# Kernel tuning notes

Hardware: AMD Instinct MI355X
Metric: run time of the kernel (lower is better)

Reference implementation:

```python
import jax, jax.numpy as jnp
import numpy as np

GELU = lambda x: jax.nn.gelu(x, approximate=False)  # torch nn.GELU default (erf)
BN_EPS = 1e-5

def _conv(x, w, pad):
    return jax.lax.conv_general_dilated(x, w, (1, 1), pad,
                                        dimension_numbers=('NCHW', 'OIHW', 'NCHW'))

def setup_inputs() -> dict:
    B, D, L = 4096, 768, 3
    IC, R = D // 2, 16  # FDA intermediate channels, reduction ratio
    ks = iter(jax.random.split(jax.random.key(0), 64))
    def nrm(shape, s=0.02):
        return jax.random.normal(next(ks), shape, jnp.float32) * s
    z = lambda *s: jnp.zeros(s, jnp.float32)
    o = lambda *s: jnp.ones(s, jnp.float32)
    inp = {
        'text_feature': jax.random.normal(next(ks), (B, D), jnp.float32),
        'image_feature': jax.random.normal(next(ks), (B, D), jnp.float32),
        'tl_w': nrm((D, D)), 'tl_b': z(D),
        'il_w': nrm((D, D)), 'il_b': z(D),
        'sda_wq': nrm((512, D)), 'sda_bq': z(512),
        'sda_wk': nrm((512, D)), 'sda_bk': z(512),
        'sda_wv': nrm((512, D)), 'sda_bv': z(512),
        'sda_wo': nrm((D, 512)), 'sda_bo': z(D),
        'fda_w1': nrm((IC, D, 3, 3)), 'fda_b1': z(IC),
        'fda_bn1_g': o(IC), 'fda_bn1_b': z(IC),
        'fda_ca_w1': nrm((IC // R, IC, 1, 1)), 'fda_ca_w2': nrm((IC, IC // R, 1, 1)),
        'fda_sa_w': nrm((1, IC, 7, 7)), 'fda_sa_b': z(1),
        'fda_dec_w': nrm((1, IC, 1, 1)), 'fda_dec_b': z(1),
        'fda_sigma': jnp.full((1, IC, 1, 1), 1e-5, jnp.float32),
        'fda_wf': nrm((D, IC, 1, 1)), 'fda_bf': z(D),
        'fda_bn2_g': o(D), 'fda_bn2_b': z(D),
        'dmi_wq': nrm((D, D)), 'dmi_bq': z(D),
        'dmi_wk': nrm((D, D)), 'dmi_bk': z(D),
        'dmi_wv': nrm((D, D)), 'dmi_bv': z(D),
        'tg_w1': nrm((D, D)), 'tg_b1': z(D),
        'tg_w2': nrm((D, D)), 'tg_b2': z(D),
        'ig_w1': nrm((D, D)), 'ig_b1': z(D),
        'ig_w2': nrm((D, D)), 'ig_b2': z(D),
        'text_scale': o(1, D), 'image_scale': o(1, D),
        'cls_w': nrm((L, D)), 'cls_b': z(L),
    }
    return inp

def reference(text_feature, image_feature, tl_w, tl_b, il_w, il_b,
              sda_wq, sda_bq, sda_wk, sda_bk, sda_wv, sda_bv, sda_wo, sda_bo,
              fda_w1, fda_b1, fda_bn1_g, fda_bn1_b, fda_ca_w1, fda_ca_w2,
              fda_sa_w, fda_sa_b, fda_dec_w, fda_dec_b, fda_sigma,
              fda_wf, fda_bf, fda_bn2_g, fda_bn2_b,
              dmi_wq, dmi_bq, dmi_wk, dmi_bk, dmi_wv, dmi_bv,
              tg_w1, tg_b1, tg_w2, tg_b2, ig_w1, ig_b1, ig_w2, ig_b2,
              text_scale, image_scale, cls_w, cls_b):
    B, D = text_feature.shape
    H, DK = 8, 64
    # text/image projections (+GELU; dropout is identity at inference)
    t = GELU(text_feature @ tl_w.T + tl_b)
    im = GELU(image_feature @ il_w.T + il_b)
    # SDA multi-head self-attention on text, seq len 1
    q = (t @ sda_wq.T + sda_bq).reshape(B, 1, H, DK).transpose(0, 2, 1, 3)  # [B,H,1,DK]
    k = (t @ sda_wk.T + sda_bk).reshape(B, 1, H, DK).transpose(0, 2, 1, 3)
    v = (t @ sda_wv.T + sda_bv).reshape(B, 1, H, DK).transpose(0, 2, 1, 3)
    att = jax.nn.softmax(jnp.einsum('bhqd,bhkd->bhqk', q, k) / jnp.sqrt(jnp.float32(DK)), -1)
    t = jnp.einsum('bhqk,bhkd->bhqd', att, v).transpose(0, 2, 1, 3).reshape(B, H * DK) @ sda_wo.T + sda_bo
    # FDA on image feature viewed as [B,C,1,1]
    bnscale = 1.0 / jnp.sqrt(1.0 + BN_EPS)  # BN eval mode, running_mean=0, running_var=1
    x = im[:, :, None, None]
    x = _conv(x, fda_w1, ((1, 1), (1, 1))) + fda_b1[None, :, None, None]
    x = GELU(x * bnscale * fda_bn1_g[None, :, None, None] + fda_bn1_b[None, :, None, None])
    ca = jnp.mean(x, axis=(2, 3), keepdims=True)  # AdaptiveAvgPool2d(1)
    ca = GELU(_conv(ca, fda_ca_w1, ((0, 0), (0, 0))))
    ca = jax.nn.sigmoid(_conv(ca, fda_ca_w2, ((0, 0), (0, 0))))
    x = x * ca
    sa = jax.nn.sigmoid(_conv(x, fda_sa_w, ((3, 3), (3, 3))) + fda_sa_b[None, :, None, None])
    x = x * sa
    xg = GELU(_conv(x, fda_dec_w, ((0, 0), (0, 0))) + fda_dec_b[None, :, None, None])  # [B,1,1,1]
    x = x + fda_sigma * (x - xg)  # feat_decompose residual with learned sigma
    x = _conv(x, fda_wf, ((0, 0), (0, 0))) + fda_bf[None, :, None, None]
    x = GELU(x * bnscale * fda_bn2_g[None, :, None, None] + fda_bn2_b[None, :, None, None])
    im = x[:, :, 0, 0]

    def dmi(q_in, kv_in, gw1, gb1, gw2, gb2, scale):
        qp = q_in @ dmi_wq.T + dmi_bq
        kp = kv_in @ dmi_wk.T + dmi_bk
        vp = kv_in @ dmi_wv.T + dmi_bv
        # cross-batch attention: scores are [B,B]
        a = jax.nn.softmax(qp @ kp.T / jnp.sqrt(jnp.float32(D)), -1) @ vp
        # gate Sequential ends in Sigmoid, then forward applies sigmoid AGAIN (faithful)
        gate = jax.nn.sigmoid(jax.nn.relu(a @ gw1.T + gb1) @ gw2.T + gb2)
        return jax.nn.sigmoid(gate) * a * scale

    ct = dmi(t, im, tg_w1, tg_b1, tg_w2, tg_b2, text_scale)
    ci = dmi(im, t, ig_w1, ig_b1, ig_w2, ig_b2, image_scale)
    logits = (ct + ci) @ cls_w.T + cls_b
    return jax.nn.softmax(logits, -1)
```

## Files before the change

### kernel.cpp

```cpp
#include <hip/hip_runtime.h>
#include <hip/hip_bf16.h>
#include <math.h>

typedef __hip_bfloat16 bf16;
typedef __bf16 bf16x8 __attribute__((ext_vector_type(8)));
typedef float f32x4 __attribute__((ext_vector_type(4)));
typedef unsigned short u16;
typedef u16 u16x8 __attribute__((ext_vector_type(8)));

#define NB 4096
#define DM 768

__device__ __forceinline__ float cvt(float x){ return x; }
__device__ __forceinline__ float cvt(bf16 x){ return __bfloat162float(x); }
__device__ __forceinline__ void stv(float* p, float v){ *p = v; }
__device__ __forceinline__ void stv(bf16* p, float v){ *p = __float2bfloat16(v); }

__device__ __forceinline__ float gelu_f(float x){
    return 0.5f * x * (1.0f + erff(x * 0.70710678118654752440f));
}
__device__ __forceinline__ float sigmoid_f(float x){
    return 1.0f / (1.0f + __expf(-x));
}

__device__ __forceinline__ void async_copy16(const void* g, void* l){
    __builtin_amdgcn_global_load_lds((const __attribute__((address_space(1))) void*)g,
                                     (__attribute__((address_space(3))) void*)l, 16, 0, 0);
}

#define MAXJ 8
struct Job {
    const bf16* A; const bf16* B; bf16* C;
    const float* b0; const float* gv; const float* b1;
    float* rs;
    const bf16* aux; const float* sv;
    int M, N, K, ldA, ldB, act, trans, blk0, nx, nb;
    float alpha;
};
struct Jobs { Job j[MAXJ]; int nj; };

__global__ __launch_bounds__(256) void mgemm_k(Jobs jb)
{
    int z = 0;
    #pragma unroll
    for (int i = 1; i < MAXJ; ++i)
        if (i < jb.nj && (int)blockIdx.x >= jb.j[i].blk0) z = i;
    const Job& J = jb.j[z];
    const bf16* __restrict__ A  = J.A;
    const bf16* __restrict__ Bm = J.B;
    bf16* __restrict__ C        = J.C;
    const int bx0 = (int)blockIdx.x - J.blk0;
    int bx = bx0;
    if (J.nx <= 16 && (J.nb & 7) == 0){ const int cpx = J.nb >> 3; bx = (bx0 & 7) * cpx + (bx0 >> 3); }
    const int gx = bx % J.nx;
    const int gy = bx / J.nx;
    const int M = J.M, N = J.N, K = J.K, ldA = J.ldA, ldB = J.ldB;

    __shared__ __align__(16) bf16 smem[17408];
    const int tid  = threadIdx.x;
    const int wave = tid >> 6;
    const int lane = tid & 63;
    const int row0 = gy * 128;
    const int col0 = gx * 128;
    const int wrow = (wave & 1) * 64;
    const int wcol = (wave >> 1) * 64;
    const int fl   = lane & 15;
    const int q    = lane >> 4;

    const int sr8 = lane >> 3;
    const int sc8 = (((lane & 7) ^ sr8)) * 8;
    const bf16* pA = A  + (size_t)(row0 + wave * 32 + sr8) * ldA + sc8;
    const bf16* pB = Bm + (size_t)(col0 + wave * 32 + sr8) * ldB + sc8;
    bf16* ldsA = &smem[(wave * 32) * 64];
    bf16* ldsB = &smem[8192 + (wave * 32) * 64];

    f32x4 acc[4][4] = {};
    for (int k0 = 0; k0 < K; k0 += 64){
        #pragma unroll
        for (int i = 0; i < 4; ++i){
            async_copy16(pA + (size_t)(i * 8) * ldA, ldsA + i * 512);
            async_copy16(pB + (size_t)(i * 8) * ldB, ldsB + i * 512);
        }
        pA += 64; pB += 64;
        __syncthreads();
        #pragma unroll
        for (int ks = 0; ks < 2; ++ks){
            bf16x8 af[4], bfv[4];
            #pragma unroll
            for (int i = 0; i < 4; ++i){
                const int ra = wrow + i * 16 + fl;
                const int rb = wcol + i * 16 + fl;
                const int ca = ((ks * 4 + q) ^ (ra & 7)) * 8;
                const int cb = ((ks * 4 + q) ^ (rb & 7)) * 8;
                af[i]  = *(const bf16x8*)&smem[ra * 64 + ca];
                bfv[i] = *(const bf16x8*)&smem[8192 + rb * 64 + cb];
            }
            #pragma unroll
            for (int mi = 0; mi < 4; ++mi)
                #pragma unroll
                for (int ni = 0; ni < 4; ++ni)
                    acc[mi][ni] = __builtin_amdgcn_mfma_f32_16x16x32_bf16(af[mi], bfv[ni], acc[mi][ni], 0, 0, 0);
        }
        __syncthreads();
    }

    constexpr int ELD = 136;
    #pragma unroll
    for (int ni = 0; ni < 4; ++ni){
        const int col = col0 + wcol + ni * 16 + fl;
        const float b0 = J.b0 ? J.b0[col] : 0.f;
        const float gm = (J.gv ? J.gv[col] : 1.f) * J.alpha;
        const float b1 = J.b1 ? J.b1[col] : 0.f;
        const int lcol = wcol + ni * 16 + fl;
        #pragma unroll
        for (int mi = 0; mi < 4; ++mi){
            const int lrow = wrow + mi * 16 + q * 4;
            #pragma unroll
            for (int r = 0; r < 4; ++r){
                float v = (acc[mi][ni][r] + b0) * gm + b1;
                if      (J.act == 1) v = gelu_f(v);
                else if (J.act == 2) v = sigmoid_f(v);
                else if (J.act == 3) v = fmaxf(v, 0.f);
                else if (J.act == 4) v = __expf(v);
                if (J.trans) smem[(size_t)lcol * ELD + lrow + r] = __float2bfloat16(v);
                else         smem[(size_t)(lrow + r) * ELD + lcol] = __float2bfloat16(v);
            }
        }
    }
    __syncthreads();
    const int erow = tid >> 4;
    const int ecol = (tid & 15) * 8;
    #pragma unroll
    for (int p = 0; p < 8; ++p){
        const int row = p * 16 + erow;
        u16x8 uv = *(const u16x8*)&smem[row * ELD + ecol];
        if (J.act == 5){
            const u16x8 av = *(const u16x8*)((const u16*)J.aux + (size_t)(row0 + row) * N + col0 + ecol);
            #pragma unroll
            for (int j = 0; j < 8; ++j){
                const float g = __uint_as_float((unsigned)uv[j] << 16);
                const float a = __uint_as_float((unsigned)av[j] << 16);
                const float v = sigmoid_f(g) * a * J.sv[col0 + ecol + j];
                uv[j] = __bfloat16_as_ushort(__float2bfloat16(v));
            }
        }
        if (J.trans) *(u16x8*)&C[(size_t)(col0 + row) * M + row0 + ecol] = uv;
        else         *(u16x8*)&C[(size_t)(row0 + row) * N + col0 + ecol] = uv;
        if (J.rs){
            float s = 0.f;
            #pragma unroll
            for (int j = 0; j < 8; ++j) s += __uint_as_float((unsigned)uv[j] << 16);
            s += __shfl_down(s, 8, 16);
            s += __shfl_down(s, 4, 16);
            s += __shfl_down(s, 2, 16);
            s += __shfl_down(s, 1, 16);
            if ((tid & 15) == 0) J.rs[(size_t)gx * M + row0 + row] = s;
        }
    }
}

__global__ __launch_bounds__(256) void denom_k(const float* __restrict__ part, float* __restrict__ l)
{
    const int t = blockIdx.x * 256 + threadIdx.x;
    if (t >= 2 * NB) return;
    const int dir = t >> 12, row = t & (NB - 1);
    const float* p = part + (size_t)dir * 32 * NB + row;
    float s = 0.f;
    #pragma unroll
    for (int c = 0; c < 32; ++c) s += p[(size_t)c * NB];
    l[t] = s;
}

#define NCVT 14
struct CvtDesc { const float* s[NCVT]; bf16* d[NCVT]; int n[NCVT]; };
__global__ __launch_bounds__(256) void cvt_k(CvtDesc cd,
    const float* __restrict__ w1, const float* __restrict__ saw,
    bf16* __restrict__ w1c, float* __restrict__ sac,
    const float* __restrict__ bq, const float* __restrict__ bk,
    float* __restrict__ qkb)
{
    const int e = blockIdx.y;
    if (e == NCVT){
        const int idx = blockIdx.x * 256 + threadIdx.x;
        if (idx < 384 * 768){
            const int oc = idx / 768, ic = idx % 768;
            w1c[idx] = __float2bfloat16(w1[(size_t)oc * 6912 + (size_t)ic * 9 + 4]);
        }
        if (idx < 384) sac[idx] = saw[(size_t)idx * 49 + 24];
        if (idx < 768)                   qkb[idx] = bq[idx];
        else if (idx < 1536)             qkb[idx] = bk[idx - 768];
        return;
    }
    const int base = (blockIdx.x * 256 + threadIdx.x) * 4;
    if (base >= cd.n[e]) return;
    const float4 v = *(const float4*)(cd.s[e] + base);
    union { bf16 h[4]; unsigned long long u; } o;
    o.h[0] = __float2bfloat16(v.x);
    o.h[1] = __float2bfloat16(v.y);
    o.h[2] = __float2bfloat16(v.z);
    o.h[3] = __float2bfloat16(v.w);
    *(unsigned long long*)(cd.d[e] + base) = o.u;
}

__global__ __launch_bounds__(128) void fda_fused_k(
    bf16* __restrict__ x, const float* __restrict__ wc1, const float* __restrict__ wc2,
    const float* __restrict__ sac, const float* __restrict__ sab,
    const float* __restrict__ decw, const float* __restrict__ decb,
    const float* __restrict__ sigma)
{
    __shared__ float xs[384];
    __shared__ float ca1s[24];
    __shared__ float red[128];
    const int b = blockIdx.x;
    const int tid = threadIdx.x;
    bf16* xr = x + (size_t)b * 384;
    #pragma unroll
    for (int i = 0; i < 3; ++i) xs[tid + i * 128] = cvt(xr[tid + i * 128]);
    __syncthreads();
    if (tid < 96){
        const int o = tid >> 2, sub = tid & 3;
        const float* w = wc1 + (size_t)o * 384 + sub * 96;
        float p = 0.f;
        #pragma unroll 8
        for (int k = 0; k < 96; ++k) p = fmaf(xs[sub * 96 + k], w[k], p);
        p += __shfl_down(p, 1, 64);
        p += __shfl_down(p, 2, 64);
        if (sub == 0) ca1s[o] = gelu_f(p);
    }
    __syncthreads();
    float x2[3];
    float p = 0.f;
    #pragma unroll
    for (int i = 0; i < 3; ++i){
        const int c = tid + i * 128;
        float s = 0.f;
        const float* w = wc2 + (size_t)c * 24;
        #pragma unroll
        for (int k = 0; k < 24; ++k) s = fmaf(ca1s[k], w[k], s);
        const float v = xs[c] * sigmoid_f(s);
        x2[i] = v;
        p += v * sac[c];
    }
    red[tid] = p; __syncthreads();
    for (int s = 64; s > 0; s >>= 1){ if (tid < s) red[tid] += red[tid + s]; __syncthreads(); }
    const float sa = sigmoid_f(red[0] + sab[0]);
    __syncthreads();
    float qq = 0.f;
    #pragma unroll
    for (int i = 0; i < 3; ++i){
        const int c = tid + i * 128;
        x2[i] *= sa;
        qq += x2[i] * decw[c];
    }
    red[tid] = qq; __syncthreads();
    for (int s = 64; s > 0; s >>= 1){ if (tid < s) red[tid] += red[tid + s]; __syncthreads(); }
    const float xg = gelu_f(red[0] + decb[0]);
    #pragma unroll
    for (int i = 0; i < 3; ++i){
        const int c = tid + i * 128;
        const float sg = sigma[c];
        stv(&xr[c], x2[i] + sg * (x2[i] - xg));
    }
}

__global__ __launch_bounds__(256) void reduce2_k(
    const bf16* __restrict__ a, const bf16* __restrict__ b, bf16* __restrict__ o1,
    const float* __restrict__ l1,
    const bf16* __restrict__ c, const bf16* __restrict__ d, bf16* __restrict__ o2,
    const float* __restrict__ l2)
{
    const size_t i = ((size_t)blockIdx.x * 256 + threadIdx.x) * 8;
    if (i >= (size_t)NB * DM) return;
    const int row = (int)(i / DM);
    const float inv1 = 1.0f / l1[row];
    const float inv2 = 1.0f / l2[row];
    u16x8 ua = *(const u16x8*)((const u16*)a + i);
    u16x8 ub = *(const u16x8*)((const u16*)b + i);
    u16x8 uc = *(const u16x8*)((const u16*)c + i);
    u16x8 ud = *(const u16x8*)((const u16*)d + i);
    u16x8 r1, r2;
    #pragma unroll
    for (int j = 0; j < 8; ++j){
        const float s1 = (__uint_as_float((unsigned)ua[j] << 16) + __uint_as_float((unsigned)ub[j] << 16)) * inv1;
        const float s2 = (__uint_as_float((unsigned)uc[j] << 16) + __uint_as_float((unsigned)ud[j] << 16)) * inv2;
        r1[j] = __bfloat16_as_ushort(__float2bfloat16(s1));
        r2[j] = __bfloat16_as_ushort(__float2bfloat16(s2));
    }
    *(u16x8*)((u16*)o1 + i) = r1;
    *(u16x8*)((u16*)o2 + i) = r2;
}

__global__ __launch_bounds__(256) void combine_cls_k(
    const bf16* __restrict__ v1, const bf16* __restrict__ v2,
    const float* __restrict__ w, const float* __restrict__ bias, float* __restrict__ out)
{
    __shared__ float r0[256], r1[256], r2[256];
    const int b = blockIdx.x;
    const int tid = threadIdx.x;
    const size_t off = (size_t)b * DM;
    float p0 = 0.f, p1 = 0.f, p2 = 0.f;
    #pragma unroll
    for (int i = 0; i < 3; ++i){
        const int c = tid + i * 256;
        const float v = cvt(v1[off + c]) + cvt(v2[off + c]);
        p0 = fmaf(v, w[c],         p0);
        p1 = fmaf(v, w[DM + c],    p1);
        p2 = fmaf(v, w[2*DM + c],  p2);
    }
    r0[tid] = p0; r1[tid] = p1; r2[tid] = p2; __syncthreads();
    for (int s = 128; s > 0; s >>= 1){
        if (tid < s){ r0[tid] += r0[tid + s]; r1[tid] += r1[tid + s]; r2[tid] += r2[tid + s]; }
        __syncthreads();
    }
    if (tid == 0){
        const float l0 = r0[0] + bias[0];
        const float l1 = r1[0] + bias[1];
        const float l2 = r2[0] + bias[2];
        const float mx = fmaxf(l0, fmaxf(l1, l2));
        const float e0 = __expf(l0 - mx), e1 = __expf(l1 - mx), e2 = __expf(l2 - mx);
        const float inv = 1.f / (e0 + e1 + e2);
        out[(size_t)b * 3 + 0] = e0 * inv;
        out[(size_t)b * 3 + 1] = e1 * inv;
        out[(size_t)b * 3 + 2] = e2 * inv;
    }
}

extern "C" void kernel_launch(void* const* d_in, const int* in_sizes, int n_in,
                              void* d_out, int out_size, void* d_ws, size_t ws_size,
                              hipStream_t stream)
{
    const float* text   = (const float*)d_in[0];
    const float* image  = (const float*)d_in[1];
    const float* tl_w   = (const float*)d_in[2];
    const float* tl_b   = (const float*)d_in[3];
    const float* il_w   = (const float*)d_in[4];
    const float* il_b   = (const float*)d_in[5];
    const float* sda_wv = (const float*)d_in[10];
    const float* sda_bv = (const float*)d_in[11];
    const float* sda_wo = (const float*)d_in[12];
    const float* sda_bo = (const float*)d_in[13];
    const float* fda_w1 = (const float*)d_in[14];
    const float* fda_b1 = (const float*)d_in[15];
    const float* bn1_g  = (const float*)d_in[16];
    const float* bn1_b  = (const float*)d_in[17];
    const float* ca_w1  = (const float*)d_in[18];
    const float* ca_w2  = (const float*)d_in[19];
    const float* sa_w   = (const float*)d_in[20];
    const float* sa_b   = (const float*)d_in[21];
    const float* dec_w  = (const float*)d_in[22];
    const float* dec_b  = (const float*)d_in[23];
    const float* sigma  = (const float*)d_in[24];
    const float* fda_wf = (const float*)d_in[25];
    const float* fda_bf = (const float*)d_in[26];
    const float* bn2_g  = (const float*)d_in[27];
    const float* bn2_b  = (const float*)d_in[28];
    const float* dmi_wq = (const float*)d_in[29];
    const float* dmi_bq = (const float*)d_in[30];
    const float* dmi_wk = (const float*)d_in[31];
    const float* dmi_bk = (const float*)d_in[32];
    const float* dmi_wv = (const float*)d_in[33];
    const float* dmi_bv = (const float*)d_in[34];
    const float* tg_w1  = (const float*)d_in[35];
    const float* tg_b1  = (const float*)d_in[36];
    const float* tg_w2  = (const float*)d_in[37];
    const float* tg_b2  = (const float*)d_in[38];
    const float* ig_w1  = (const float*)d_in[39];
    const float* ig_b1  = (const float*)d_in[40];
    const float* ig_w2  = (const float*)d_in[41];
    const float* ig_b2  = (const float*)d_in[42];
    const float* t_scale= (const float*)d_in[43];
    const float* i_scale= (const float*)d_in[44];
    const float* cls_w  = (const float*)d_in[45];
    const float* cls_b  = (const float*)d_in[46];
    float* out = (float*)d_out;

    char* base = (char*)d_ws;
    auto alloc = [&](size_t bytes){ void* p = (void*)base; base += (bytes + 255) & ~(size_t)255; return p; };
    const size_t SLOT = (size_t)NB * DM;
    const size_t W768 = (size_t)768 * 768;
    bf16* tl_wb   = (bf16*)alloc(W768 * 2);
    bf16* il_wb   = (bf16*)alloc(W768 * 2);
    bf16* sda_wvb = (bf16*)alloc((size_t)512 * 768 * 2);
    bf16* sda_wob = (bf16*)alloc((size_t)768 * 512 * 2);
    bf16* fda_wfb = (bf16*)alloc((size_t)768 * 384 * 2);
    bf16* dmi_wqb = (bf16*)alloc(W768 * 2);
    bf16* dmi_wkb = (bf16*)alloc(W768 * 2);
    bf16* dmi_wvb = (bf16*)alloc(W768 * 2);
    bf16* tg_w1b  = (bf16*)alloc(W768 * 2);
    bf16* tg_w2b  = (bf16*)alloc(W768 * 2);
    bf16* ig_w1b  = (bf16*)alloc(W768 * 2);
    bf16* ig_w2b  = (bf16*)alloc(W768 * 2);
    bf16* w1c     = (bf16*)alloc((size_t)384 * 768 * 2);
    float* sac    = (float*)alloc(1536 * 4);
    float* qkb    = (float*)alloc(1536 * 4);
    float* lbuf   = (float*)alloc(2 * NB * 4);
    float* part   = (float*)alloc((size_t)2 * 32 * NB * 4);
    bf16* SL[8];
    for (int i = 0; i < 8; ++i) SL[i] = (bf16*)alloc(SLOT * 2);
    bf16* SC1 = (bf16*)alloc((size_t)NB * NB * 2);
    bf16* SC2 = (bf16*)alloc((size_t)NB * NB * 2);

    const float bnscale = 1.0f / sqrtf(1.0f + 1e-5f);
    const float iscale  = 1.0f / sqrtf(768.0f);
    const dim3 blk(256);

    struct JB {
        Jobs jb; int blocks;
        void add(const bf16* A, const bf16* B, bf16* C, int M, int N, int K, int ldA, int ldB,
                 const float* b0, float al, const float* gv, const float* b1, int act, int trans,
                 float* rs = nullptr, const bf16* aux = nullptr, const float* sv = nullptr){
            Job& j = jb.j[jb.nj++];
            j.A=A; j.B=B; j.C=C; j.b0=b0; j.gv=gv; j.b1=b1; j.rs=rs; j.aux=aux; j.sv=sv;
            j.M=M; j.N=N; j.K=K; j.ldA=ldA; j.ldB=ldB; j.act=act; j.trans=trans;
            j.alpha=al; j.blk0=blocks; j.nx=N/128; j.nb=(N/128)*(M/128);
            blocks += (N/128)*(M/128);
        }
    };
    auto launch = [&](JB& b){ mgemm_k<<<dim3(b.blocks), blk, 0, stream>>>(b.jb); };

    CvtDesc cd;
    const float* srcs[NCVT] = {text, image, tl_w, il_w, sda_wv, sda_wo, fda_wf,
                               dmi_wq, dmi_wk, dmi_wv, tg_w1, tg_w2, ig_w1, ig_w2};
    bf16* dsts[NCVT] = {SL[0], SL[1], tl_wb, il_wb, sda_wvb, sda_wob, fda_wfb,
                        dmi_wqb, dmi_wkb, dmi_wvb, tg_w1b, tg_w2b, ig_w1b, ig_w2b};
    int   lens[NCVT] = {(int)SLOT, (int)SLOT, (int)W768, (int)W768, 512*768, 768*512, 768*384,
                        (int)W768, (int)W768, (int)W768, (int)W768, (int)W768, (int)W768, (int)W768};
    for (int i = 0; i < NCVT; ++i){ cd.s[i] = srcs[i]; cd.d[i] = dsts[i]; cd.n[i] = lens[i]; }
    cvt_k<<<dim3((int)(SLOT / 1024), NCVT + 1), blk, 0, stream>>>(cd, fda_w1, sa_w, w1c, sac,
                                                                  dmi_bq, dmi_bk, qkb);

    { JB b{}; b.add(SL[0], tl_wb, SL[2], NB, DM, DM, DM, DM, tl_b, 1.f, nullptr, nullptr, 1, 0);
              b.add(SL[1], il_wb, SL[3], NB, DM, DM, DM, DM, il_b, 1.f, nullptr, nullptr, 1, 0); launch(b); }
    { JB b{}; b.add(SL[2], sda_wvb, SL[0], NB, 512, DM, DM, DM, sda_bv, 1.f, nullptr, nullptr, 0, 0);
              b.add(SL[3], w1c,     SL[1], NB, 384, DM, DM, DM, fda_b1, bnscale, bn1_g, bn1_b, 1, 0); launch(b); }
    fda_fused_k<<<dim3(NB), dim3(128), 0, stream>>>(SL[1], ca_w1, ca_w2, sac, sa_b, dec_w, dec_b, sigma);
    { JB b{}; b.add(SL[0], sda_wob, SL[4], NB, DM, 512, 512, 512, sda_bo, 1.f, nullptr, nullptr, 0, 0);
              b.add(SL[1], fda_wfb, SL[5], NB, DM, 384, 384, 384, fda_bf, bnscale, bn2_g, bn2_b, 1, 0); launch(b); }

    { JB b{};
      b.add(SL[4], dmi_wqb, SL[0], NB, 1536, DM, DM, DM, qkb,    1.f, nullptr, nullptr, 0, 0);
      b.add(SL[5], dmi_wqb, SL[2], NB, 1536, DM, DM, DM, qkb,    1.f, nullptr, nullptr, 0, 0);
      b.add(SL[5], dmi_wvb, SL[6], NB, DM,   DM, DM, DM, dmi_bv, 1.f, nullptr, nullptr, 0, 1);
      b.add(SL[4], dmi_wvb, SL[7], NB, DM,   DM, DM, DM, dmi_bv, 1.f, nullptr, nullptr, 0, 1);
      launch(b); }
    { JB b{}; b.add(SL[0],       SL[2] + 768, SC1, NB, NB, DM, 1536, 1536, nullptr, iscale, nullptr, nullptr, 4, 0, part);
              b.add(SL[2],       SL[0] + 768, SC2, NB, NB, DM, 1536, 1536, nullptr, iscale, nullptr, nullptr, 4, 0, part + 32 * NB); launch(b); }
    denom_k<<<dim3((2 * NB + 255) / 256), blk, 0, stream>>>(part, lbuf);
    { JB b{};
      b.add(SC1,        SL[6],        SL[0], NB, DM, 2048, NB, NB, nullptr, 1.f, nullptr, nullptr, 0, 0);
      b.add(SC1 + 2048, SL[6] + 2048, SL[1], NB, DM, 2048, NB, NB, nullptr, 1.f, nullptr, nullptr, 0, 0);
      b.add(SC2,        SL[7],        SL[2], NB, DM, 2048, NB, NB, nullptr, 1.f, nullptr, nullptr, 0, 0);
      b.add(SC2 + 2048, SL[7] + 2048, SL[3], NB, DM, 2048, NB, NB, nullptr, 1.f, nullptr, nullptr, 0, 0);
      launch(b); }
    reduce2_k<<<dim3((int)(SLOT / 2048)), blk, 0, stream>>>(SL[0], SL[1], SL[4], lbuf,
                                                           SL[2], SL[3], SL[5], lbuf + NB);
    { JB b{}; b.add(SL[4], tg_w1b, SL[0], NB, DM, DM, DM, DM, tg_b1, 1.f, nullptr, nullptr, 3, 0);
              b.add(SL[5], ig_w1b, SL[1], NB, DM, DM, DM, DM, ig_b1, 1.f, nullptr, nullptr, 3, 0); launch(b); }
    { JB b{}; b.add(SL[0], tg_w2b, SL[3], NB, DM, DM, DM, DM, tg_b2, 1.f, nullptr, nullptr, 5, 0, nullptr, SL[4], t_scale);
              b.add(SL[1], ig_w2b, SL[6], NB, DM, DM, DM, DM, ig_b2, 1.f, nullptr, nullptr, 5, 0, nullptr, SL[5], i_scale); launch(b); }
    combine_cls_k<<<dim3(NB), blk, 0, stream>>>(SL[3], SL[6], cls_w, cls_b, out);
}
```

Measured before the change: 539.1 us.

## Fuse classifier dot products into gate GEMM epilogue and split Q/K outputs

The final gate GEMM epilogue now computes per-tile partial dot products against the three classifier rows and writes them to a small partial buffer instead of storing the bf16 gated outputs. A tiny finishing kernel sums the 12 partials per row and applies softmax, replacing the per-row combine kernel that re-read two full activation tensors. Separately, the Q/K projection writes its K half into a separate contiguous buffer, so the score GEMM reads B with leading dimension 768 instead of 1536. This trades a larger epilogue (extra cw loads and shuffles) for less global traffic and one lighter launch.

Measured after the change: 553.9 us. 2.7% more time.

```diff
diff --git a/kernel.cpp b/kernel.cpp
--- a/kernel.cpp
+++ b/kernel.cpp
@@ -30,10 +30,11 @@
 
 #define MAXJ 8
 struct Job {
-    const bf16* A; const bf16* B; bf16* C;
+    const bf16* A; const bf16* B; bf16* C; bf16* C2;
     const float* b0; const float* gv; const float* b1;
     float* rs;
     const bf16* aux; const float* sv;
+    const float* cw; float* rs3;
     int M, N, K, ldA, ldB, act, trans, blk0, nx, nb;
     float alpha;
 };
@@ -128,6 +129,8 @@
         }
     }
     __syncthreads();
+    bf16* Cd = C; int ccol0 = col0; int ldC = N;
+    if (J.C2){ ldC = N >> 1; if (col0 >= ldC){ Cd = J.C2; ccol0 = col0 - ldC; } }
     const int erow = tid >> 4;
     const int ecol = (tid & 15) * 8;
     #pragma unroll
@@ -136,16 +139,37 @@
         u16x8 uv = *(const u16x8*)&smem[row * ELD + ecol];
         if (J.act == 5){
             const u16x8 av = *(const u16x8*)((const u16*)J.aux + (size_t)(row0 + row) * N + col0 + ecol);
+            float vv[8];
             #pragma unroll
             for (int j = 0; j < 8; ++j){
                 const float g = __uint_as_float((unsigned)uv[j] << 16);
                 const float a = __uint_as_float((unsigned)av[j] << 16);
-                const float v = sigmoid_f(g) * a * J.sv[col0 + ecol + j];
-                uv[j] = __bfloat16_as_ushort(__float2bfloat16(v));
+                vv[j] = sigmoid_f(g) * a * J.sv[col0 + ecol + j];
+                uv[j] = __bfloat16_as_ushort(__float2bfloat16(vv[j]));
             }
-        }
-        if (J.trans) *(u16x8*)&C[(size_t)(col0 + row) * M + row0 + ecol] = uv;
-        else         *(u16x8*)&C[(size_t)(row0 + row) * N + col0 + ecol] = uv;
+            if (J.cw){
+                float s0 = 0.f, s1 = 0.f, s2 = 0.f;
+                #pragma unroll
+                for (int j = 0; j < 8; ++j){
+                    const int c = col0 + ecol + j;
+                    s0 = fmaf(vv[j], J.cw[c],          s0);
+                    s1 = fmaf(vv[j], J.cw[DM + c],     s1);
+                    s2 = fmaf(vv[j], J.cw[2 * DM + c], s2);
+                }
+                s0 += __shfl_down(s0, 8, 16); s1 += __shfl_down(s1, 8, 16); s2 += __shfl_down(s2, 8, 16);
+                s0 += __shfl_down(s0, 4, 16); s1 += __shfl_down(s1, 4, 16); s2 += __shfl_down(s2, 4, 16);
+                s0 += __shfl_down(s0, 2, 16); s1 += __shfl_down(s1, 2, 16); s2 += __shfl_down(s2, 2, 16);
+                s0 += __shfl_down(s0, 1, 16); s1 += __shfl_down(s1, 1, 16); s2 += __shfl_down(s2, 1, 16);
+                if ((tid & 15) == 0){
+                    float* d = J.rs3 + ((size_t)gx * M + row0 + row) * 3;
+                    d[0] = s0; d[1] = s1; d[2] = s2;
+                }
+            }
+        }
+        if (!(J.act == 5 && J.cw)){
+            if (J.trans) *(u16x8*)&C[(size_t)(col0 + row) * M + row0 + ecol] = uv;
+            else         *(u16x8*)&Cd[(size_t)(row0 + row) * ldC + ccol0 + ecol] = uv;
+        }
         if (J.rs){
             float s = 0.f;
             #pragma unroll
@@ -290,39 +314,23 @@
     *(u16x8*)((u16*)o2 + i) = r2;
 }
 
-__global__ __launch_bounds__(256) void combine_cls_k(
-    const bf16* __restrict__ v1, const bf16* __restrict__ v2,
-    const float* __restrict__ w, const float* __restrict__ bias, float* __restrict__ out)
-{
-    __shared__ float r0[256], r1[256], r2[256];
-    const int b = blockIdx.x;
-    const int tid = threadIdx.x;
-    const size_t off = (size_t)b * DM;
-    float p0 = 0.f, p1 = 0.f, p2 = 0.f;
-    #pragma unroll
-    for (int i = 0; i < 3; ++i){
-        const int c = tid + i * 256;
-        const float v = cvt(v1[off + c]) + cvt(v2[off + c]);
-        p0 = fmaf(v, w[c],         p0);
-        p1 = fmaf(v, w[DM + c],    p1);
-        p2 = fmaf(v, w[2*DM + c],  p2);
-    }
-    r0[tid] = p0; r1[tid] = p1; r2[tid] = p2; __syncthreads();
-    for (int s = 128; s > 0; s >>= 1){
-        if (tid < s){ r0[tid] += r0[tid + s]; r1[tid] += r1[tid + s]; r2[tid] += r2[tid + s]; }
-        __syncthreads();
-    }
-    if (tid == 0){
-        const float l0 = r0[0] + bias[0];
-        const float l1 = r1[0] + bias[1];
-        const float l2 = r2[0] + bias[2];
-        const float mx = fmaxf(l0, fmaxf(l1, l2));
-        const float e0 = __expf(l0 - mx), e1 = __expf(l1 - mx), e2 = __expf(l2 - mx);
-        const float inv = 1.f / (e0 + e1 + e2);
-        out[(size_t)b * 3 + 0] = e0 * inv;
-        out[(size_t)b * 3 + 1] = e1 * inv;
-        out[(size_t)b * 3 + 2] = e2 * inv;
-    }
+__global__ __launch_bounds__(256) void cls_fin_k(
+    const float* __restrict__ p2, const float* __restrict__ bias, float* __restrict__ out)
+{
+    const int row = blockIdx.x * 256 + threadIdx.x;
+    if (row >= NB) return;
+    float l0 = bias[0], l1 = bias[1], l2 = bias[2];
+    #pragma unroll
+    for (int g = 0; g < 12; ++g){
+        const float* q = p2 + ((size_t)g * NB + row) * 3;
+        l0 += q[0]; l1 += q[1]; l2 += q[2];
+    }
+    const float mx = fmaxf(l0, fmaxf(l1, l2));
+    const float e0 = __expf(l0 - mx), e1 = __expf(l1 - mx), e2 = __expf(l2 - mx);
+    const float inv = 1.f / (e0 + e1 + e2);
+    out[(size_t)row * 3 + 0] = e0 * inv;
+    out[(size_t)row * 3 + 1] = e1 * inv;
+    out[(size_t)row * 3 + 2] = e2 * inv;
 }
 
 extern "C" void kernel_launch(void* const* d_in, const int* in_sizes, int n_in,
@@ -395,6 +403,7 @@
     float* qkb    = (float*)alloc(1536 * 4);
     float* lbuf   = (float*)alloc(2 * NB * 4);
     float* part   = (float*)alloc((size_t)2 * 32 * NB * 4);
+    float* part2  = (float*)alloc((size_t)12 * NB * 3 * 4);
     bf16* SL[8];
     for (int i = 0; i < 8; ++i) SL[i] = (bf16*)alloc(SLOT * 2);
     bf16* SC1 = (bf16*)alloc((size_t)NB * NB * 2);
@@ -408,9 +417,11 @@
         Jobs jb; int blocks;
         void add(const bf16* A, const bf16* B, bf16* C, int M, int N, int K, int ldA, int ldB,
                  const float* b0, float al, const float* gv, const float* b1, int act, int trans,
-                 float* rs = nullptr, const bf16* aux = nullptr, const float* sv = nullptr){
+                 float* rs = nullptr, const bf16* aux = nullptr, const float* sv = nullptr,
+                 bf16* C2 = nullptr, const float* cw = nullptr, float* rs3 = nullptr){
             Job& j = jb.j[jb.nj++];
-            j.A=A; j.B=B; j.C=C; j.b0=b0; j.gv=gv; j.b1=b1; j.rs=rs; j.aux=aux; j.sv=sv;
+            j.A=A; j.B=B; j.C=C; j.C2=C2; j.b0=b0; j.gv=gv; j.b1=b1; j.rs=rs; j.aux=aux; j.sv=sv;
+            j.cw=cw; j.rs3=rs3;
             j.M=M; j.N=N; j.K=K; j.ldA=ldA; j.ldB=ldB; j.act=act; j.trans=trans;
             j.alpha=al; j.blk0=blocks; j.nx=N/128; j.nb=(N/128)*(M/128);
             blocks += (N/128)*(M/128);
@@ -438,13 +449,15 @@
               b.add(SL[1], fda_wfb, SL[5], NB, DM, 384, 384, 384, fda_bf, bnscale, bn2_g, bn2_b, 1, 0); launch(b); }
 
     { JB b{};
-      b.add(SL[4], dmi_wqb, SL[0], NB, 1536, DM, DM, DM, qkb,    1.f, nullptr, nullptr, 0, 0);
-      b.add(SL[5], dmi_wqb, SL[2], NB, 1536, DM, DM, DM, qkb,    1.f, nullptr, nullptr, 0, 0);
+      b.add(SL[4], dmi_wqb, SL[0], NB, 1536, DM, DM, DM, qkb,    1.f, nullptr, nullptr, 0, 0,
+            nullptr, nullptr, nullptr, SL[1]);
+      b.add(SL[5], dmi_wqb, SL[2], NB, 1536, DM, DM, DM, qkb,    1.f, nullptr, nullptr, 0, 0,
+            nullptr, nullptr, nullptr, SL[3]);
       b.add(SL[5], dmi_wvb, SL[6], NB, DM,   DM, DM, DM, dmi_bv, 1.f, nullptr, nullptr, 0, 1);
       b.add(SL[4], dmi_wvb, SL[7], NB, DM,   DM, DM, DM, dmi_bv, 1.f, nullptr, nullptr, 0, 1);
       launch(b); }
-    { JB b{}; b.add(SL[0],       SL[2] + 768, SC1, NB, NB, DM, 1536, 1536, nullptr, iscale, nullptr, nullptr, 4, 0, part);
-              b.add(SL[2],       SL[0] + 768, SC2, NB, NB, DM, 1536, 1536, nullptr, iscale, nullptr, nullptr, 4, 0, part + 32 * NB); launch(b); }
+    { JB b{}; b.add(SL[0], SL[3], SC1, NB, NB, DM, DM, DM, nullptr, iscale, nullptr, nullptr, 4, 0, part);
+              b.add(SL[2], SL[1], SC2, NB, NB, DM, DM, DM, nullptr, iscale, nullptr, nullptr, 4, 0, part + 32 * NB); launch(b); }
     denom_k<<<dim3((2 * NB + 255) / 256), blk, 0, stream>>>(part, lbuf);
     { JB b{};
       b.add(SC1,        SL[6],        SL[0], NB, DM, 2048, NB, NB, nullptr, 1.f, nullptr, nullptr, 0, 0);
@@ -456,7 +469,9 @@
                                                            SL[2], SL[3], SL[5], lbuf + NB);
     { JB b{}; b.add(SL[4], tg_w1b, SL[0], NB, DM, DM, DM, DM, tg_b1, 1.f, nullptr, nullptr, 3, 0);
               b.add(SL[5], ig_w1b, SL[1], NB, DM, DM, DM, DM, ig_b1, 1.f, nullptr, nullptr, 3, 0); launch(b); }
-    { JB b{}; b.add(SL[0], tg_w2b, SL[3], NB, DM, DM, DM, DM, tg_b2, 1.f, nullptr, nullptr, 5, 0, nullptr, SL[4], t_scale);
-              b.add(SL[1], ig_w2b, SL[6], NB, DM, DM, DM, DM, ig_b2, 1.f, nullptr, nullptr, 5, 0, nullptr, SL[5], i_scale); launch(b); }
-    combine_cls_k<<<dim3(NB), blk, 0, stream>>>(SL[3], SL[6], cls_w, cls_b, out);
-}
+    { JB b{}; b.add(SL[0], tg_w2b, SL[3], NB, DM, DM, DM, DM, tg_b2, 1.f, nullptr, nullptr, 5, 0,
+                    nullptr, SL[4], t_scale, nullptr, cls_w, part2);
+              b.add(SL[1], ig_w2b, SL[6], NB, DM, DM, DM, DM, ig_b2, 1.f, nullptr, nullptr, 5, 0,
+                    nullptr, SL[5], i_scale, nullptr, cls_w, part2 + (size_t)6 * NB * 3); launch(b); }
+    cls_fin_k<<<dim3((NB + 255) / 256), blk, 0, stream>>>(part2, cls_b, out);
+}
```
